# Performance work log

Hardware: AMD Instinct MI355X
Metric: run time of the kernel (lower is better)

## Reference

```python
import jax, jax.numpy as jnp
from jax import lax
import numpy as np

B, L_IN, C_IN, C_MARK = 4, 1024, 7, 4
D, H, DK, DFF, NL = 512, 8, 64, 2048, 4
WINDOW = [4, 4, 4]
INNER = 5


def _get_mask(input_size, window_size, inner_size):
    all_size = [input_size]
    for w in window_size:
        all_size.append(all_size[-1] // w)
    L = sum(all_size)
    m = np.zeros((L, L), dtype=np.float32)
    iw = inner_size // 2
    for li in range(len(all_size)):
        start = sum(all_size[:li])
        for i in range(start, start + all_size[li]):
            m[i, max(i - iw, start):min(i + iw + 1, start + all_size[li])] = 1
    for li in range(1, len(all_size)):
        start = sum(all_size[:li])
        for i in range(start, start + all_size[li]):
            ls = start - all_size[li - 1] + (i - start) * window_size[li - 1]
            if i == start + all_size[li] - 1:
                rs = start
            else:
                rs = start - all_size[li - 1] + (i - start + 1) * window_size[li - 1]
            m[i, ls:rs] = 1
            m[ls:rs, i] = 1
    return (1 - m).astype(bool), all_size


def _refer_points(all_sizes, window_size):
    n = all_sizes[0]
    idx = np.zeros((n, len(all_sizes)), dtype=np.int64)
    for i in range(n):
        idx[i, 0] = i
        former = i
        for j in range(1, len(all_sizes)):
            start = sum(all_sizes[:j])
            inner = former - (start - all_sizes[j - 1])
            former = start + min(inner // window_size[j - 1], all_sizes[j] - 1)
            idx[i, j] = former
    return idx


def _pos_emb(L, d):
    pos = np.arange(L, dtype=np.float32)[:, None]
    div = np.exp(np.arange(0, d, 2, dtype=np.float32) * (-np.log(10000.0) / d))
    pe = np.zeros((L, d), dtype=np.float32)
    pe[:, 0::2] = np.sin(pos * div)
    pe[:, 1::2] = np.cos(pos * div)
    return pe


def _ln(x, g, b, eps=1e-5):
    mu = x.mean(-1, keepdims=True)
    v = ((x - mu) ** 2).mean(-1, keepdims=True)
    return (x - mu) * lax.rsqrt(v + eps) * g + b


def setup_inputs() -> dict:
    key = jax.random.key(0)
    ks = iter(jax.random.split(key, 64))

    def nrm(shape, fan_in):
        return jax.random.normal(next(ks), shape, jnp.float32) / np.float32(np.sqrt(fan_in))

    return dict(
        x_enc=jax.random.normal(next(ks), (B, L_IN, C_IN), jnp.float32),
        x_mark=jax.random.uniform(next(ks), (B, L_IN, C_MARK), jnp.float32),
        conv_w=nrm((D, C_IN, 3), C_IN * 3), conv_b=jnp.zeros((D,), jnp.float32),
        temp_w=nrm((C_MARK, D), C_MARK), temp_b=jnp.zeros((D,), jnp.float32),
        down_w=nrm((D, DK), D), down_b=jnp.zeros((DK,), jnp.float32),
        pyr_conv_w=nrm((3, DK, DK, WINDOW[0]), DK * WINDOW[0]),
        pyr_conv_b=jnp.zeros((3, DK), jnp.float32),
        bn_g=jnp.ones((3, DK), jnp.float32), bn_b=jnp.zeros((3, DK), jnp.float32),
        up_w=nrm((DK, D), DK), up_b=jnp.zeros((D,), jnp.float32),
        norm_g=jnp.ones((D,), jnp.float32), norm_b=jnp.zeros((D,), jnp.float32),
        wq=nrm((NL, D, H * DK), D), wk=nrm((NL, D, H * DK), D), wv=nrm((NL, D, H * DK), D),
        fc_w=nrm((NL, H * DK, D), H * DK), fc_b=jnp.zeros((NL, D), jnp.float32),
        ln1_g=jnp.ones((NL, D), jnp.float32), ln1_b=jnp.zeros((NL, D), jnp.float32),
        w1=nrm((NL, D, DFF), D), b1=jnp.zeros((NL, DFF), jnp.float32),
        w2=nrm((NL, DFF, D), DFF), b2=jnp.zeros((NL, D), jnp.float32),
        ln2_g=jnp.ones((NL, D), jnp.float32), ln2_b=jnp.zeros((NL, D), jnp.float32),
    )


def reference(x_enc, x_mark, conv_w, conv_b, temp_w, temp_b, down_w, down_b,
              pyr_conv_w, pyr_conv_b, bn_g, bn_b, up_w, up_b, norm_g, norm_b,
              wq, wk, wv, fc_w, fc_b, ln1_g, ln1_b, w1, b1, w2, b2, ln2_g, ln2_b):
    mask_np, all_size = _get_mask(L_IN, WINDOW, INNER)
    mask = jnp.asarray(mask_np)                      # (L_tot, L_tot) bool, True = blocked
    idx = jnp.asarray(_refer_points(all_size, WINDOW))  # (L_IN, n_levels)
    pe = jnp.asarray(_pos_emb(L_IN, D))
    L_tot = sum(all_size)

    # --- DataEmbedding: circular Conv1d token emb + positional + temporal linear ---
    xt = jnp.transpose(x_enc, (0, 2, 1))             # (B, C_IN, L)
    xt = jnp.concatenate([xt[:, :, -1:], xt, xt[:, :, :1]], axis=-1)  # circular pad=1
    val = lax.conv_general_dilated(xt, conv_w, (1,), 'VALID',
                                   dimension_numbers=('NCH', 'OIH', 'NCH'))
    val = jnp.transpose(val, (0, 2, 1)) + conv_b
    seq = val + pe[None] + x_mark @ temp_w + temp_b  # (B, L_IN, D); dropout = eval no-op

    # --- Bottleneck_Construct: build pyramid levels with strided convs ---
    tmp = jnp.transpose(seq @ down_w + down_b, (0, 2, 1))  # (B, DK, L_IN)
    outs = []
    for i in range(len(WINDOW)):
        tmp = lax.conv_general_dilated(tmp, pyr_conv_w[i], (WINDOW[i],), 'VALID',
                                       dimension_numbers=('NCH', 'OIH', 'NCH'))
        tmp = tmp + pyr_conv_b[i][None, :, None]
        # BatchNorm1d at eval with running stats (0,1): affine only
        tmp = jax.nn.elu(tmp * bn_g[i][None, :, None] + bn_b[i][None, :, None])
        outs.append(tmp)
    pyr = jnp.transpose(jnp.concatenate(outs, axis=2), (0, 2, 1)) @ up_w + up_b
    seq = _ln(jnp.concatenate([seq, pyr], axis=1), norm_g, norm_b)  # (B, L_tot, D)

    temperature = float(np.sqrt(DK))
    for l in range(NL):
        # post-norm multi-head attention with pyramidal boolean mask
        res = seq
        q = (seq @ wq[l]).reshape(B, L_tot, H, DK)
        k = (seq @ wk[l]).reshape(B, L_tot, H, DK)
        v = (seq @ wv[l]).reshape(B, L_tot, H, DK)
        att = jnp.einsum('bqhd,bkhd->bhqk', q / temperature, k)
        att = jnp.where(mask[None, None], jnp.float32(-1e9), att)
        p = jax.nn.softmax(att, axis=-1)
        o = jnp.einsum('bhqk,bkhd->bqhd', p, v).reshape(B, L_tot, H * DK)
        seq = _ln(o @ fc_w[l] + fc_b[l] + res, ln1_g[l], ln1_b[l])
        # post-norm FFN (exact gelu, as F.gelu)
        res = seq
        hmid = jax.nn.gelu(seq @ w1[l] + b1[l], approximate=False)
        seq = _ln(hmid @ w2[l] + b2[l] + res, ln2_g[l], ln2_b[l])

    # --- refer_points gather: concat all pyramid levels per input position ---
    out = seq[:, idx, :]                             # (B, L_IN, n_levels, D)
    return out.reshape(B, L_IN, -1)                  # (B, L_IN, n_levels*D)
```

## Files before the change

### kernel.cpp

```cpp
#include <hip/hip_runtime.h>
#include <hip/hip_bf16.h>
#include <math.h>


typedef __attribute__((ext_vector_type(8))) short short8;
typedef __attribute__((ext_vector_type(4))) float f32x4;

__device__ inline ushort f2bf(float x) {
  union { __hip_bfloat16 h; ushort u; } cv; cv.h = __float2bfloat16(x); return cv.u;
}
__device__ inline float bf2f(ushort u) {
  union { unsigned int i; float f; } cv; cv.i = (unsigned)u << 16; return cv.f;
}
__device__ inline float lo16(unsigned u) { union { unsigned i; float f; } c; c.i = u << 16; return c.f; }
__device__ inline float hi16(unsigned u) { union { unsigned i; float f; } c; c.i = u & 0xffff0000u; return c.f; }

__device__ inline float gelu_f(float x) {
  float y = 0.7978845608028654f * (x + 0.044715f * x * x * x);
  float t = __expf(-2.0f * y);
  float th = (1.0f - t) / (1.0f + t);
  return 0.5f * x * (1.0f + th);
}

__device__ inline int xcd_chunk(int orig, int nwg) {
  int q = nwg >> 3, r = nwg & 7;
  int xcd = orig & 7, idx = orig >> 3;
  int base = (xcd < r) ? xcd * (q + 1) : r * (q + 1) + (xcd - r) * q;
  return base + idx;
}

#define GLD16(gp, lp)                                                        \
  __builtin_amdgcn_global_load_lds(                                          \
      (const __attribute__((address_space(1))) void*)(gp),                   \
      (__attribute__((address_space(3))) void*)(lp), 16, 0, 0)

__global__ __launch_bounds__(512) void embed_kernel(
    const float* __restrict__ x_enc, const float* __restrict__ x_mark,
    const float* __restrict__ conv_w, const float* __restrict__ conv_b,
    const float* __restrict__ temp_w, const float* __restrict__ temp_b,
    float* __restrict__ e) {
  int bl = blockIdx.x;
  int b = bl >> 10, l = bl & 1023;
  int d = threadIdx.x;
  int lm1 = (l + 1023) & 1023;
  int lp1 = (l + 1) & 1023;
  const float* w  = conv_w + d * 21;
  const float* x0 = x_enc + (size_t)(b * 1024 + lm1) * 7;
  const float* x1 = x_enc + (size_t)(b * 1024 + l)   * 7;
  const float* x2 = x_enc + (size_t)(b * 1024 + lp1) * 7;
  float acc = conv_b[d];
#pragma unroll
  for (int ci = 0; ci < 7; ci++) {
    acc = fmaf(x0[ci], w[ci * 3 + 0], acc);
    acc = fmaf(x1[ci], w[ci * 3 + 1], acc);
    acc = fmaf(x2[ci], w[ci * 3 + 2], acc);
  }
  int j = d >> 1;
  float dv = expf((float)(2 * j) * (-9.210340371976184f / 512.0f));
  float ang = (float)l * dv;
  float pe = (d & 1) ? cosf(ang) : sinf(ang);
  const float* xm = x_mark + (size_t)(b * 1024 + l) * 4;
  float mk = temp_b[d];
  mk = fmaf(xm[0], temp_w[d],        mk);
  mk = fmaf(xm[1], temp_w[512 + d],  mk);
  mk = fmaf(xm[2], temp_w[1024 + d], mk);
  mk = fmaf(xm[3], temp_w[1536 + d], mk);
  e[(size_t)bl * 512 + d] = acc + pe + mk;
}

__global__ __launch_bounds__(256) void transpose_cast(
    const float* __restrict__ src, ushort* __restrict__ dst,
    int K, int N, size_t src_lstride, size_t dst_lstride) {
  src += (size_t)blockIdx.z * src_lstride;
  dst += (size_t)blockIdx.z * dst_lstride;
  __shared__ float t[32][33];
  int k0 = blockIdx.y * 32, n0 = blockIdx.x * 32;
  int tx = threadIdx.x, ty = threadIdx.y;
#pragma unroll
  for (int i = 0; i < 4; i++)
    t[ty + i * 8][tx] = src[(size_t)(k0 + ty + i * 8) * N + n0 + tx];
  __syncthreads();
#pragma unroll
  for (int i = 0; i < 4; i++)
    dst[(size_t)(n0 + ty + i * 8) * K + k0 + tx] = f2bf(t[tx][ty + i * 8]);
}

__global__ __launch_bounds__(256) void gemm_bf16(
    const ushort* __restrict__ A, const ushort* __restrict__ Bt,
    const float* __restrict__ bias, void* __restrict__ C,
    int N, int K, int act, int out_bf16) {
  __shared__ short As[2][4096];
  __shared__ short Bs[2][8192];
  int nbx = N >> 7;
  int wgid = xcd_chunk(blockIdx.x, gridDim.x);
  int bx = wgid % nbx, by = wgid / nbx;
  int tid = threadIdx.x;
  int w = tid >> 6, lane = tid & 63;
  int bm = by << 6, bn = bx << 7;
  int gch = (tid & 7) ^ ((tid >> 3) & 7);
  const short* Ab = (const short*)A + (size_t)(bm + (tid >> 3)) * K + gch * 8;
  const short* Bb = (const short*)Bt + (size_t)(bn + (tid >> 3)) * K + gch * 8;
  int ldst = (tid & 192) * 8;
  int wr = (w >> 1) << 5, wc = (w & 1) << 6;
  int lr = lane & 15, kg = lane >> 4;
  int cs0 = ((kg)     ^ (lane & 7)) * 8;
  int cs1 = ((4 + kg) ^ (lane & 7)) * 8;
  f32x4 acc[2][4] = {};
#define STG(buf, kt)  do {                                                   \
    GLD16(Ab + (kt),                      &As[buf][ldst]);                   \
    GLD16(Ab + (kt) + (size_t)32 * K,     &As[buf][2048 + ldst]);            \
    GLD16(Bb + (kt),                      &Bs[buf][ldst]);                   \
    GLD16(Bb + (kt) + (size_t)32 * K,     &Bs[buf][2048 + ldst]);            \
    GLD16(Bb + (kt) + (size_t)64 * K,     &Bs[buf][4096 + ldst]);            \
    GLD16(Bb + (kt) + (size_t)96 * K,     &Bs[buf][6144 + ldst]); } while (0)
  STG(0, 0);
  __syncthreads();
  int nt = K >> 6;
  for (int t = 0; t < nt; t++) {
    int cur = t & 1;
    if (t + 1 < nt) STG(cur ^ 1, (t + 1) << 6);
    short8 a_[2][2], b_[4][2];
#pragma unroll
    for (int m = 0; m < 2; m++) {
      int rb = (wr + m * 16 + lr) * 64;
      a_[m][0] = *(const short8*)&As[cur][rb + cs0];
      a_[m][1] = *(const short8*)&As[cur][rb + cs1];
    }
#pragma unroll
    for (int n = 0; n < 4; n++) {
      int rb = (wc + n * 16 + lr) * 64;
      b_[n][0] = *(const short8*)&Bs[cur][rb + cs0];
      b_[n][1] = *(const short8*)&Bs[cur][rb + cs1];
    }
#pragma unroll
    for (int ks = 0; ks < 2; ks++)
#pragma unroll
      for (int m = 0; m < 2; m++)
#pragma unroll
        for (int n = 0; n < 4; n++)
          acc[m][n] = __builtin_amdgcn_mfma_f32_16x16x32_bf16(a_[m][ks], b_[n][ks], acc[m][n], 0, 0, 0);
    __syncthreads();
  }
#undef STG
  int r0 = bm + wr + kg * 4;
  int c0 = bn + wc + lr;
#pragma unroll
  for (int m = 0; m < 2; m++) {
#pragma unroll
    for (int n = 0; n < 4; n++) {
      int col = c0 + n * 16;
      float bv = bias ? bias[col] : 0.0f;
#pragma unroll
      for (int j = 0; j < 4; j++) {
        int row = r0 + m * 16 + j;
        float v = acc[m][n][j] + bv;
        if (act == 1) v = gelu_f(v);
        if (out_bf16) ((ushort*)C)[(size_t)row * N + col] = f2bf(v);
        else          ((float*)C)[(size_t)row * N + col] = v;
      }
    }
  }
}

__global__ __launch_bounds__(256) void gemm_bf16_t64(
    const ushort* __restrict__ A, const ushort* __restrict__ Bt,
    const float* __restrict__ bias, void* __restrict__ C,
    int N, int K, int out_bf16) {
  __shared__ short As[2][4096];
  __shared__ short Bs[2][4096];
  int nbx = N >> 6;
  int wgid = xcd_chunk(blockIdx.x, gridDim.x);
  int bx = wgid % nbx, by = wgid / nbx;
  int tid = threadIdx.x;
  int w = tid >> 6, lane = tid & 63;
  int bm = by << 6, bn = bx << 6;
  int gch = (tid & 7) ^ ((tid >> 3) & 7);
  const short* Ab = (const short*)A + (size_t)(bm + (tid >> 3)) * K + gch * 8;
  const short* Bb = (const short*)Bt + (size_t)(bn + (tid >> 3)) * K + gch * 8;
  int ldst = (tid & 192) * 8;
  int wr = (w >> 1) << 5, wc = (w & 1) << 5;
  int lr = lane & 15, kg = lane >> 4;
  int cs0 = ((kg)     ^ (lane & 7)) * 8;
  int cs1 = ((4 + kg) ^ (lane & 7)) * 8;
  f32x4 acc[2][2] = {};
#define STG64(buf, kt) do {                                                  \
    GLD16(Ab + (kt),                  &As[buf][ldst]);                       \
    GLD16(Ab + (kt) + (size_t)32 * K, &As[buf][2048 + ldst]);                \
    GLD16(Bb + (kt),                  &Bs[buf][ldst]);                       \
    GLD16(Bb + (kt) + (size_t)32 * K, &Bs[buf][2048 + ldst]); } while (0)
  STG64(0, 0);
  __syncthreads();
  int nt = K >> 6;
  for (int t = 0; t < nt; t++) {
    int cur = t & 1;
    if (t + 1 < nt) STG64(cur ^ 1, (t + 1) << 6);
    short8 a_[2][2], b_[2][2];
#pragma unroll
    for (int m = 0; m < 2; m++) {
      int rb = (wr + m * 16 + lr) * 64;
      a_[m][0] = *(const short8*)&As[cur][rb + cs0];
      a_[m][1] = *(const short8*)&As[cur][rb + cs1];
    }
#pragma unroll
    for (int n = 0; n < 2; n++) {
      int rb = (wc + n * 16 + lr) * 64;
      b_[n][0] = *(const short8*)&Bs[cur][rb + cs0];
      b_[n][1] = *(const short8*)&Bs[cur][rb + cs1];
    }
#pragma unroll
    for (int ks = 0; ks < 2; ks++)
#pragma unroll
      for (int m = 0; m < 2; m++)
#pragma unroll
        for (int n = 0; n < 2; n++)
          acc[m][n] = __builtin_amdgcn_mfma_f32_16x16x32_bf16(a_[m][ks], b_[n][ks], acc[m][n], 0, 0, 0);
    __syncthreads();
  }
#undef STG64
  int r0 = bm + wr + kg * 4;
  int c0 = bn + wc + lr;
#pragma unroll
  for (int m = 0; m < 2; m++) {
#pragma unroll
    for (int n = 0; n < 2; n++) {
      int col = c0 + n * 16;
      float bv = bias ? bias[col] : 0.0f;
#pragma unroll
      for (int j = 0; j < 4; j++) {
        int row = r0 + m * 16 + j;
        float v = acc[m][n][j] + bv;
        if (out_bf16) ((ushort*)C)[(size_t)row * N + col] = f2bf(v);
        else          ((float*)C)[(size_t)row * N + col] = v;
      }
    }
  }
}

__global__ __launch_bounds__(256) void down_gemm(
    const float* __restrict__ A, const float* __restrict__ B,
    const float* __restrict__ bias, float* __restrict__ C) {
  int wgid = xcd_chunk(blockIdx.x, gridDim.x);
  int r0 = wgid << 4;
  int tid = threadIdx.x;
  int col = tid & 63, rq = tid >> 6;
  __shared__ float As[16][32];
  __shared__ float Bs[32][64];
  float acc0 = 0, acc1 = 0, acc2 = 0, acc3 = 0;
  for (int kt = 0; kt < 512; kt += 32) {
    {
      int e = tid * 2;
      int ar = e >> 5, ak = e & 31;
      *(float2*)&As[ar][ak] = *(const float2*)&A[(size_t)(r0 + ar) * 512 + kt + ak];
    }
    {
      int e = tid * 8;
      int br = e >> 6, bc = e & 63;
      *(float4*)&Bs[br][bc]     = *(const float4*)&B[(size_t)(kt + br) * 64 + bc];
      *(float4*)&Bs[br][bc + 4] = *(const float4*)&B[(size_t)(kt + br) * 64 + bc + 4];
    }
    __syncthreads();
#pragma unroll
    for (int kk = 0; kk < 32; kk++) {
      float bv = Bs[kk][col];
      acc0 = fmaf(As[rq][kk],      bv, acc0);
      acc1 = fmaf(As[rq + 4][kk],  bv, acc1);
      acc2 = fmaf(As[rq + 8][kk],  bv, acc2);
      acc3 = fmaf(As[rq + 12][kk], bv, acc3);
    }
    __syncthreads();
  }
  float bv = bias[col];
  C[(size_t)(r0 + rq) * 64 + col]      = acc0 + bv;
  C[(size_t)(r0 + rq + 4) * 64 + col]  = acc1 + bv;
  C[(size_t)(r0 + rq + 8) * 64 + col]  = acc2 + bv;
  C[(size_t)(r0 + rq + 12) * 64 + col] = acc3 + bv;
}

__global__ __launch_bounds__(256) void gemm_f32(
    const float* __restrict__ A, const float* __restrict__ B,
    const float* __restrict__ bias, float* __restrict__ C,
    int M, int N, int K) {
  __shared__ float As[16][68];
  __shared__ float Bs[16][64];
  int tid = threadIdx.x;
  int tx = tid & 15, ty = tid >> 4;
  int bm = blockIdx.y << 6, bn = blockIdx.x << 6;
  const float* Ab = A + (size_t)bm * K;
  const float* Bb = B + bn;
  float acc[4][4] = {};
  for (int kt = 0; kt < K; kt += 16) {
#pragma unroll
    for (int r = 0; r < 4; r++) {
      int e2 = r * 256 + tid;
      As[e2 & 15][e2 >> 4] = Ab[(size_t)(e2 >> 4) * K + kt + (e2 & 15)];
    }
#pragma unroll
    for (int r = 0; r < 4; r++) {
      int e2 = r * 256 + tid;
      Bs[e2 >> 6][e2 & 63] = Bb[(size_t)(kt + (e2 >> 6)) * N + (e2 & 63)];
    }
    __syncthreads();
#pragma unroll
    for (int kk = 0; kk < 16; kk++) {
      float a0 = As[kk][(ty << 2) + 0], a1 = As[kk][(ty << 2) + 1];
      float a2 = As[kk][(ty << 2) + 2], a3 = As[kk][(ty << 2) + 3];
      float b0 = Bs[kk][(tx << 2) + 0], b1 = Bs[kk][(tx << 2) + 1];
      float b2 = Bs[kk][(tx << 2) + 2], b3 = Bs[kk][(tx << 2) + 3];
      acc[0][0] = fmaf(a0, b0, acc[0][0]); acc[0][1] = fmaf(a0, b1, acc[0][1]);
      acc[0][2] = fmaf(a0, b2, acc[0][2]); acc[0][3] = fmaf(a0, b3, acc[0][3]);
      acc[1][0] = fmaf(a1, b0, acc[1][0]); acc[1][1] = fmaf(a1, b1, acc[1][1]);
      acc[1][2] = fmaf(a1, b2, acc[1][2]); acc[1][3] = fmaf(a1, b3, acc[1][3]);
      acc[2][0] = fmaf(a2, b0, acc[2][0]); acc[2][1] = fmaf(a2, b1, acc[2][1]);
      acc[2][2] = fmaf(a2, b2, acc[2][2]); acc[2][3] = fmaf(a2, b3, acc[2][3]);
      acc[3][0] = fmaf(a3, b0, acc[3][0]); acc[3][1] = fmaf(a3, b1, acc[3][1]);
      acc[3][2] = fmaf(a3, b2, acc[3][2]); acc[3][3] = fmaf(a3, b3, acc[3][3]);
    }
    __syncthreads();
  }
#pragma unroll
  for (int i2 = 0; i2 < 4; i2++) {
    int row = bm + (ty << 2) + i2;
#pragma unroll
    for (int j2 = 0; j2 < 4; j2++) {
      int col = bn + (tx << 2) + j2;
      C[(size_t)row * N + col] = acc[i2][j2] + (bias ? bias[col] : 0.0f);
    }
  }
}

__global__ __launch_bounds__(64) void pyr_conv(
    const float* __restrict__ in, int in_base, int in_bstr,
    float* __restrict__ out, int out_base, int out_bstr, int out_len,
    const float* __restrict__ w, const float* __restrict__ bias,
    const float* __restrict__ bng, const float* __restrict__ bnb) {
  int blk = blockIdx.x;
  int b = blk / out_len, to = blk - b * out_len;
  int co = threadIdx.x;
  __shared__ float xin[4][64];
  const float* src = in + (size_t)(b * in_bstr + in_base + 4 * to) * 64;
#pragma unroll
  for (int r2 = 0; r2 < 4; r2++) xin[r2][co] = src[r2 * 64 + co];
  __syncthreads();
  const float* wr = w + (size_t)co * 256;
  float acc = bias[co];
#pragma unroll 16
  for (int ci = 0; ci < 64; ci++) {
    acc = fmaf(xin[0][ci], wr[ci * 4 + 0], acc);
    acc = fmaf(xin[1][ci], wr[ci * 4 + 1], acc);
    acc = fmaf(xin[2][ci], wr[ci * 4 + 2], acc);
    acc = fmaf(xin[3][ci], wr[ci * 4 + 3], acc);
  }
  float y = fmaf(bng[co], acc, bnb[co]);
  y = y > 0.0f ? y : expm1f(y);
  out[(size_t)(b * out_bstr + out_base + to) * 64 + co] = y;
}

__global__ __launch_bounds__(256) void ln_concat(
    const float* __restrict__ e, const float* __restrict__ pyru,
    const float* __restrict__ g, const float* __restrict__ bta,
    float* __restrict__ seq, ushort* __restrict__ seq_bf) {
  int r = blockIdx.x;
  int b = r / 1360, i = r - b * 1360;
  int tid = threadIdx.x;
  const float* src = (i < 1024)
      ? (e    + (size_t)(b * 1024 + i) * 512)
      : (pyru + (size_t)(b * 336 + (i - 1024)) * 512);
  float v0 = src[tid], v1 = src[tid + 256];
  __shared__ float red[256];
  red[tid] = v0 + v1;
  __syncthreads();
  for (int st = 128; st > 0; st >>= 1) { if (tid < st) red[tid] += red[tid + st]; __syncthreads(); }
  float mu = red[0] * (1.0f / 512.0f);
  __syncthreads();
  float d0 = v0 - mu, d1 = v1 - mu;
  red[tid] = d0 * d0 + d1 * d1;
  __syncthreads();
  for (int st = 128; st > 0; st >>= 1) { if (tid < st) red[tid] += red[tid + st]; __syncthreads(); }
  float inv = rsqrtf(red[0] * (1.0f / 512.0f) + 1e-5f);
  float o0 = d0 * inv * g[tid]       + bta[tid];
  float o1 = d1 * inv * g[tid + 256] + bta[tid + 256];
  float* dst = seq + (size_t)r * 512;
  dst[tid] = o0; dst[tid + 256] = o1;
  ushort* dbf = seq_bf + (size_t)r * 512;
  dbf[tid] = f2bf(o0); dbf[tid + 256] = f2bf(o1);
}

__global__ __launch_bounds__(256) void ln_add(
    float* __restrict__ seq, const ushort* __restrict__ t1,
    const float* __restrict__ g, const float* __restrict__ bta,
    ushort* __restrict__ seq_bf) {
  int r = blockIdx.x;
  int tid = threadIdx.x;
  float* row = seq + (size_t)r * 512;
  const ushort* trow = t1 + (size_t)r * 512;
  float v0 = row[tid] + bf2f(trow[tid]);
  float v1 = row[tid + 256] + bf2f(trow[tid + 256]);
  __shared__ float red[256];
  red[tid] = v0 + v1;
  __syncthreads();
  for (int st = 128; st > 0; st >>= 1) { if (tid < st) red[tid] += red[tid + st]; __syncthreads(); }
  float mu = red[0] * (1.0f / 512.0f);
  __syncthreads();
  float d0 = v0 - mu, d1 = v1 - mu;
  red[tid] = d0 * d0 + d1 * d1;
  __syncthreads();
  for (int st = 128; st > 0; st >>= 1) { if (tid < st) red[tid] += red[tid + st]; __syncthreads(); }
  float inv = rsqrtf(red[0] * (1.0f / 512.0f) + 1e-5f);
  float o0 = d0 * inv * g[tid]       + bta[tid];
  float o1 = d1 * inv * g[tid + 256] + bta[tid + 256];
  row[tid] = o0; row[tid + 256] = o1;
  ushort* dbf = seq_bf + (size_t)r * 512;
  dbf[tid] = f2bf(o0); dbf[tid + 256] = f2bf(o1);
}

__global__ __launch_bounds__(512) void attn_sparse(
    const ushort* __restrict__ qkv, ushort* __restrict__ o) {
  int r = blockIdx.x;
  int b = r / 1360, i = r - b * 1360;
  int h = threadIdx.x >> 6, lane = threadIdx.x & 63;
  int S, sz, li;
  if (i < 1024)      { li = 0; S = 0;    sz = 1024; }
  else if (i < 1280) { li = 1; S = 1024; sz = 256; }
  else if (i < 1344) { li = 2; S = 1280; sz = 64; }
  else               { li = 3; S = 1344; sz = 16; }
  int p = i - S;
  int lo = p - 2; if (lo < 0) lo = 0;
  int hi = p + 2; if (hi > sz - 1) hi = sz - 1;
  int cnt = hi - lo + 1;
  int nk = cnt + (li > 0 ? 4 : 0) + (li < 3 ? 1 : 0);
  int Sprev = (li == 1) ? 0 : (li == 2) ? 1024 : 1280;
  int Snext = (li == 0) ? 1024 : (li == 1) ? 1280 : 1344;
  int j2 = lane >> 2, c = lane & 3;
  int key;
  if (j2 < cnt)                      key = S + lo + j2;
  else if (li > 0 && j2 - cnt < 4)   key = Sprev + 4 * p + (j2 - cnt);
  else if (li < 3)                   key = Snext + (p >> 2);
  else                               key = S + p;
  float partial = 0.0f;
  {
    const uint4* qv = (const uint4*)(qkv + (size_t)r * 1536 + h * 64 + c * 16);
    const uint4* kv = (const uint4*)(qkv + (size_t)(b * 1360 + key) * 1536 + 512 + h * 64 + c * 16);
#pragma unroll
    for (int cc = 0; cc < 2; cc++) {
      uint4 a = qv[cc], k4 = kv[cc];
      partial = fmaf(lo16(a.x), lo16(k4.x), partial); partial = fmaf(hi16(a.x), hi16(k4.x), partial);
      partial = fmaf(lo16(a.y), lo16(k4.y), partial); partial = fmaf(hi16(a.y), hi16(k4.y), partial);
      partial = fmaf(lo16(a.z), lo16(k4.z), partial); partial = fmaf(hi16(a.z), hi16(k4.z), partial);
      partial = fmaf(lo16(a.w), lo16(k4.w), partial); partial = fmaf(hi16(a.w), hi16(k4.w), partial);
    }
  }
  partial += __shfl_xor(partial, 1);
  partial += __shfl_xor(partial, 2);
  float s = partial * 0.125f;
  float m = -1e30f;
  for (int j = 0; j < nk; j++) m = fmaxf(m, __shfl(s, 4 * j));
  float denom = 0.0f;
  for (int j = 0; j < nk; j++) denom += __expf(__shfl(s, 4 * j) - m);
  float inv = 1.0f / denom;
  float acc = 0.0f;
  for (int j = 0; j < nk; j++) {
    float pj = __expf(__shfl(s, 4 * j) - m) * inv;
    int kj = __shfl(key, 4 * j);
    float vv = bf2f(qkv[(size_t)(b * 1360 + kj) * 1536 + 1024 + h * 64 + lane]);
    acc = fmaf(pj, vv, acc);
  }
  o[(size_t)r * 512 + h * 64 + lane] = f2bf(acc);
}

__global__ __launch_bounds__(512) void gather_out(
    const float* __restrict__ seq, float* __restrict__ out) {
  int bl = blockIdx.x;
  int b = bl >> 10, i = bl & 1023;
  int d = threadIdx.x;
  size_t ob = (size_t)bl * 2048 + d;
  size_t base = (size_t)b * 1360;
  out[ob]        = seq[(base + i) * 512 + d];
  out[ob + 512]  = seq[(base + 1024 + (i >> 2)) * 512 + d];
  out[ob + 1024] = seq[(base + 1280 + (i >> 4)) * 512 + d];
  out[ob + 1536] = seq[(base + 1344 + (i >> 6)) * 512 + d];
}

extern "C" void kernel_launch(void* const* d_in, const int* in_sizes, int n_in,
                              void* d_out, int out_size, void* d_ws, size_t ws_size,
                              hipStream_t stream) {
  const float* x_enc   = (const float*)d_in[0];
  const float* x_mark  = (const float*)d_in[1];
  const float* conv_w  = (const float*)d_in[2];
  const float* conv_b  = (const float*)d_in[3];
  const float* temp_w  = (const float*)d_in[4];
  const float* temp_b  = (const float*)d_in[5];
  const float* down_w  = (const float*)d_in[6];
  const float* down_b  = (const float*)d_in[7];
  const float* pyr_w   = (const float*)d_in[8];
  const float* pyr_b   = (const float*)d_in[9];
  const float* bn_g    = (const float*)d_in[10];
  const float* bn_b    = (const float*)d_in[11];
  const float* up_w    = (const float*)d_in[12];
  const float* up_b    = (const float*)d_in[13];
  const float* norm_g  = (const float*)d_in[14];
  const float* norm_b  = (const float*)d_in[15];
  const float* wq      = (const float*)d_in[16];
  const float* wk      = (const float*)d_in[17];
  const float* wv      = (const float*)d_in[18];
  const float* fc_w    = (const float*)d_in[19];
  const float* fc_b    = (const float*)d_in[20];
  const float* ln1_g   = (const float*)d_in[21];
  const float* ln1_b   = (const float*)d_in[22];
  const float* w1      = (const float*)d_in[23];
  const float* b1      = (const float*)d_in[24];
  const float* w2      = (const float*)d_in[25];
  const float* b2      = (const float*)d_in[26];
  const float* ln2_g   = (const float*)d_in[27];
  const float* ln2_b   = (const float*)d_in[28];

  float* ws = (float*)d_ws;
  float*  e      = ws;
  float*  tmp0   = ws + 2097152;
  float*  pyrf   = ws + 2359296;
  float*  pyru   = ws + 2445312;
  ushort* qkv_bf = (ushort*)ws;
  ushort* o_bf   = (ushort*)(ws + 4227072);
  ushort* th_bf  = (ushort*)ws;
  ushort* t1     = (ushort*)(ws + 5636096);
  float*  seq    = ws + 8454144;
  ushort* seq_bf = (ushort*)(ws + 11272192);
  ushort* qkvw   = (ushort*)(ws + 12681216);
  ushort* fcw    = (ushort*)(ws + 14254080);
  ushort* w1t    = (ushort*)(ws + 14778368);
  ushort* w2t    = (ushort*)(ws + 16875520);

  dim3 tb(32, 8);
  transpose_cast<<<dim3(16, 16, 4), tb, 0, stream>>>(wq, qkvw,          512, 512,  262144, 786432);
  transpose_cast<<<dim3(16, 16, 4), tb, 0, stream>>>(wk, qkvw + 262144, 512, 512,  262144, 786432);
  transpose_cast<<<dim3(16, 16, 4), tb, 0, stream>>>(wv, qkvw + 524288, 512, 512,  262144, 786432);
  transpose_cast<<<dim3(16, 16, 4), tb, 0, stream>>>(fc_w, fcw,         512, 512,  262144, 262144);
  transpose_cast<<<dim3(64, 16, 4), tb, 0, stream>>>(w1, w1t,           512, 2048, 1048576, 1048576);
  transpose_cast<<<dim3(16, 64, 4), tb, 0, stream>>>(w2, w2t,           2048, 512, 1048576, 1048576);

  embed_kernel<<<4096, 512, 0, stream>>>(x_enc, x_mark, conv_w, conv_b,
                                         temp_w, temp_b, e);
  down_gemm<<<256, 256, 0, stream>>>(e, down_w, down_b, tmp0);
  pyr_conv<<<4 * 256, 64, 0, stream>>>(tmp0, 0, 1024, pyrf, 0, 336, 256,
                                       pyr_w, pyr_b, bn_g, bn_b);
  pyr_conv<<<4 * 64, 64, 0, stream>>>(pyrf, 0, 336, pyrf, 256, 336, 64,
                                      pyr_w + 16384, pyr_b + 64, bn_g + 64, bn_b + 64);
  pyr_conv<<<4 * 16, 64, 0, stream>>>(pyrf, 256, 336, pyrf, 320, 336, 16,
                                      pyr_w + 32768, pyr_b + 128, bn_g + 128, bn_b + 128);
  gemm_f32<<<dim3(8, 21), 256, 0, stream>>>(pyrf, up_w, up_b, pyru, 1344, 512, 64);
  ln_concat<<<5440, 256, 0, stream>>>(e, pyru, norm_g, norm_b, seq, seq_bf);

  for (int l = 0; l < 4; l++) {
    gemm_bf16<<<12 * 86, 256, 0, stream>>>(seq_bf, qkvw + (size_t)l * 786432,
                                           nullptr, qkv_bf, 1536, 512, 0, 1);
    attn_sparse<<<5440, 512, 0, stream>>>(qkv_bf, o_bf);
    gemm_bf16_t64<<<8 * 86, 256, 0, stream>>>(o_bf, fcw + (size_t)l * 262144,
                                              fc_b + l * 512, t1, 512, 512, 1);
    ln_add<<<5440, 256, 0, stream>>>(seq, t1, ln1_g + l * 512, ln1_b + l * 512, seq_bf);
    gemm_bf16<<<16 * 86, 256, 0, stream>>>(seq_bf, w1t + (size_t)l * 1048576,
                                           b1 + l * 2048, th_bf, 2048, 512, 1, 1);
    gemm_bf16_t64<<<8 * 86, 256, 0, stream>>>(th_bf, w2t + (size_t)l * 1048576,
                                              b2 + l * 512, t1, 512, 2048, 1);
    ln_add<<<5440, 256, 0, stream>>>(seq, t1, ln2_g + l * 512, ln2_b + l * 512, seq_bf);
  }
  gather_out<<<4096, 512, 0, stream>>>(seq, (float*)d_out);
}
```

Baseline: 619.6 us.

## Use 32-row tiles for N=512 GEMMs and wave-per-row layernorm kernels

The output-projection and FFN-down GEMMs now use a 32x64 tile instead of 64x64, doubling the workgroup count from 688 to 1376 so the GPU's compute units are better filled. The layernorm kernels now assign one 64-lane wave per row, using float4/uint4 vector loads and shuffle reductions in place of shared-memory tree reductions with many barriers. The smaller tile reloads the B operand more often per output element, and each wave does more serial work per row.

```diff
diff --git a/kernel.cpp b/kernel.cpp
--- a/kernel.cpp
+++ b/kernel.cpp
@@ -14,6 +14,9 @@
 }
 __device__ inline float lo16(unsigned u) { union { unsigned i; float f; } c; c.i = u << 16; return c.f; }
 __device__ inline float hi16(unsigned u) { union { unsigned i; float f; } c; c.i = u & 0xffff0000u; return c.f; }
+__device__ inline unsigned pack2(float a, float b) {
+  return (unsigned)f2bf(a) | ((unsigned)f2bf(b) << 16);
+}
 
 __device__ inline float gelu_f(float x) {
   float y = 0.7978845608028654f * (x + 0.044715f * x * x * x);
@@ -162,44 +165,42 @@
   }
 }
 
-__global__ __launch_bounds__(256) void gemm_bf16_t64(
+__global__ __launch_bounds__(256) void gemm_bf16_t32(
     const ushort* __restrict__ A, const ushort* __restrict__ Bt,
-    const float* __restrict__ bias, void* __restrict__ C,
-    int N, int K, int out_bf16) {
-  __shared__ short As[2][4096];
+    const float* __restrict__ bias, ushort* __restrict__ C,
+    int N, int K) {
+  __shared__ short As[2][2048];
   __shared__ short Bs[2][4096];
   int nbx = N >> 6;
   int wgid = xcd_chunk(blockIdx.x, gridDim.x);
   int bx = wgid % nbx, by = wgid / nbx;
   int tid = threadIdx.x;
   int w = tid >> 6, lane = tid & 63;
-  int bm = by << 6, bn = bx << 6;
+  int bm = by << 5, bn = bx << 6;
   int gch = (tid & 7) ^ ((tid >> 3) & 7);
   const short* Ab = (const short*)A + (size_t)(bm + (tid >> 3)) * K + gch * 8;
   const short* Bb = (const short*)Bt + (size_t)(bn + (tid >> 3)) * K + gch * 8;
   int ldst = (tid & 192) * 8;
-  int wr = (w >> 1) << 5, wc = (w & 1) << 5;
+  int wr = (w >> 1) << 4, wc = (w & 1) << 5;
   int lr = lane & 15, kg = lane >> 4;
   int cs0 = ((kg)     ^ (lane & 7)) * 8;
   int cs1 = ((4 + kg) ^ (lane & 7)) * 8;
-  f32x4 acc[2][2] = {};
-#define STG64(buf, kt) do {                                                  \
+  f32x4 acc[2] = {};
+#define STG32(buf, kt) do {                                                  \
     GLD16(Ab + (kt),                  &As[buf][ldst]);                       \
-    GLD16(Ab + (kt) + (size_t)32 * K, &As[buf][2048 + ldst]);                \
     GLD16(Bb + (kt),                  &Bs[buf][ldst]);                       \
     GLD16(Bb + (kt) + (size_t)32 * K, &Bs[buf][2048 + ldst]); } while (0)
-  STG64(0, 0);
+  STG32(0, 0);
   __syncthreads();
   int nt = K >> 6;
   for (int t = 0; t < nt; t++) {
     int cur = t & 1;
-    if (t + 1 < nt) STG64(cur ^ 1, (t + 1) << 6);
-    short8 a_[2][2], b_[2][2];
-#pragma unroll
-    for (int m = 0; m < 2; m++) {
-      int rb = (wr + m * 16 + lr) * 64;
-      a_[m][0] = *(const short8*)&As[cur][rb + cs0];
-      a_[m][1] = *(const short8*)&As[cur][rb + cs1];
+    if (t + 1 < nt) STG32(cur ^ 1, (t + 1) << 6);
+    short8 a_[2], b_[2][2];
+    {
+      int rb = (wr + lr) * 64;
+      a_[0] = *(const short8*)&As[cur][rb + cs0];
+      a_[1] = *(const short8*)&As[cur][rb + cs1];
     }
 #pragma unroll
     for (int n = 0; n < 2; n++) {
@@ -210,28 +211,21 @@
 #pragma unroll
     for (int ks = 0; ks < 2; ks++)
 #pragma unroll
-      for (int m = 0; m < 2; m++)
-#pragma unroll
-        for (int n = 0; n < 2; n++)
-          acc[m][n] = __builtin_amdgcn_mfma_f32_16x16x32_bf16(a_[m][ks], b_[n][ks], acc[m][n], 0, 0, 0);
+      for (int n = 0; n < 2; n++)
+        acc[n] = __builtin_amdgcn_mfma_f32_16x16x32_bf16(a_[ks], b_[n][ks], acc[n], 0, 0, 0);
     __syncthreads();
   }
-#undef STG64
+#undef STG32
   int r0 = bm + wr + kg * 4;
   int c0 = bn + wc + lr;
 #pragma unroll
-  for (int m = 0; m < 2; m++) {
-#pragma unroll
-    for (int n = 0; n < 2; n++) {
-      int col = c0 + n * 16;
-      float bv = bias ? bias[col] : 0.0f;
-#pragma unroll
-      for (int j = 0; j < 4; j++) {
-        int row = r0 + m * 16 + j;
-        float v = acc[m][n][j] + bv;
-        if (out_bf16) ((ushort*)C)[(size_t)row * N + col] = f2bf(v);
-        else          ((float*)C)[(size_t)row * N + col] = v;
-      }
+  for (int n = 0; n < 2; n++) {
+    int col = c0 + n * 16;
+    float bv = bias ? bias[col] : 0.0f;
+#pragma unroll
+    for (int j = 0; j < 4; j++) {
+      int row = r0 + j;
+      C[(size_t)row * N + col] = f2bf(acc[n][j] + bv);
     }
   }
 }
@@ -359,58 +353,79 @@
     const float* __restrict__ e, const float* __restrict__ pyru,
     const float* __restrict__ g, const float* __restrict__ bta,
     float* __restrict__ seq, ushort* __restrict__ seq_bf) {
-  int r = blockIdx.x;
+  int r = (blockIdx.x << 2) + (threadIdx.x >> 6);
+  int lane = threadIdx.x & 63;
   int b = r / 1360, i = r - b * 1360;
-  int tid = threadIdx.x;
   const float* src = (i < 1024)
       ? (e    + (size_t)(b * 1024 + i) * 512)
       : (pyru + (size_t)(b * 336 + (i - 1024)) * 512);
-  float v0 = src[tid], v1 = src[tid + 256];
-  __shared__ float red[256];
-  red[tid] = v0 + v1;
-  __syncthreads();
-  for (int st = 128; st > 0; st >>= 1) { if (tid < st) red[tid] += red[tid + st]; __syncthreads(); }
-  float mu = red[0] * (1.0f / 512.0f);
-  __syncthreads();
-  float d0 = v0 - mu, d1 = v1 - mu;
-  red[tid] = d0 * d0 + d1 * d1;
-  __syncthreads();
-  for (int st = 128; st > 0; st >>= 1) { if (tid < st) red[tid] += red[tid + st]; __syncthreads(); }
-  float inv = rsqrtf(red[0] * (1.0f / 512.0f) + 1e-5f);
-  float o0 = d0 * inv * g[tid]       + bta[tid];
-  float o1 = d1 * inv * g[tid + 256] + bta[tid + 256];
-  float* dst = seq + (size_t)r * 512;
-  dst[tid] = o0; dst[tid + 256] = o1;
-  ushort* dbf = seq_bf + (size_t)r * 512;
-  dbf[tid] = f2bf(o0); dbf[tid + 256] = f2bf(o1);
+  int c = lane << 3;
+  float4 v0 = *(const float4*)&src[c];
+  float4 v1 = *(const float4*)&src[c + 4];
+  float sum = v0.x + v0.y + v0.z + v0.w + v1.x + v1.y + v1.z + v1.w;
+#pragma unroll
+  for (int off = 1; off < 64; off <<= 1) sum += __shfl_xor(sum, off);
+  float mu = sum * (1.0f / 512.0f);
+  float d[8] = { v0.x - mu, v0.y - mu, v0.z - mu, v0.w - mu,
+                 v1.x - mu, v1.y - mu, v1.z - mu, v1.w - mu };
+  float sq = d[0]*d[0] + d[1]*d[1] + d[2]*d[2] + d[3]*d[3]
+           + d[4]*d[4] + d[5]*d[5] + d[6]*d[6] + d[7]*d[7];
+#pragma unroll
+  for (int off = 1; off < 64; off <<= 1) sq += __shfl_xor(sq, off);
+  float inv = rsqrtf(sq * (1.0f / 512.0f) + 1e-5f);
+  float4 g0 = *(const float4*)&g[c],   g1 = *(const float4*)&g[c + 4];
+  float4 b0 = *(const float4*)&bta[c], b1 = *(const float4*)&bta[c + 4];
+  float o[8] = { d[0]*inv*g0.x + b0.x, d[1]*inv*g0.y + b0.y,
+                 d[2]*inv*g0.z + b0.z, d[3]*inv*g0.w + b0.w,
+                 d[4]*inv*g1.x + b1.x, d[5]*inv*g1.y + b1.y,
+                 d[6]*inv*g1.z + b1.z, d[7]*inv*g1.w + b1.w };
+  float* dst = seq + (size_t)r * 512 + c;
+  *(float4*)&dst[0] = make_float4(o[0], o[1], o[2], o[3]);
+  *(float4*)&dst[4] = make_float4(o[4], o[5], o[6], o[7]);
+  uint4 pk;
+  pk.x = pack2(o[0], o[1]); pk.y = pack2(o[2], o[3]);
+  pk.z = pack2(o[4], o[5]); pk.w = pack2(o[6], o[7]);
+  *(uint4*)(seq_bf + (size_t)r * 512 + c) = pk;
 }
 
 __global__ __launch_bounds__(256) void ln_add(
     float* __restrict__ seq, const ushort* __restrict__ t1,
     const float* __restrict__ g, const float* __restrict__ bta,
     ushort* __restrict__ seq_bf) {
-  int r = blockIdx.x;
-  int tid = threadIdx.x;
-  float* row = seq + (size_t)r * 512;
-  const ushort* trow = t1 + (size_t)r * 512;
-  float v0 = row[tid] + bf2f(trow[tid]);
-  float v1 = row[tid + 256] + bf2f(trow[tid + 256]);
-  __shared__ float red[256];
-  red[tid] = v0 + v1;
-  __syncthreads();
-  for (int st = 128; st > 0; st >>= 1) { if (tid < st) red[tid] += red[tid + st]; __syncthreads(); }
-  float mu = red[0] * (1.0f / 512.0f);
-  __syncthreads();
-  float d0 = v0 - mu, d1 = v1 - mu;
-  red[tid] = d0 * d0 + d1 * d1;
-  __syncthreads();
-  for (int st = 128; st > 0; st >>= 1) { if (tid < st) red[tid] += red[tid + st]; __syncthreads(); }
-  float inv = rsqrtf(red[0] * (1.0f / 512.0f) + 1e-5f);
-  float o0 = d0 * inv * g[tid]       + bta[tid];
-  float o1 = d1 * inv * g[tid + 256] + bta[tid + 256];
-  row[tid] = o0; row[tid + 256] = o1;
-  ushort* dbf = seq_bf + (size_t)r * 512;
-  dbf[tid] = f2bf(o0); dbf[tid + 256] = f2bf(o1);
+  int r = (blockIdx.x << 2) + (threadIdx.x >> 6);
+  int lane = threadIdx.x & 63;
+  int c = lane << 3;
+  float* row = seq + (size_t)r * 512 + c;
+  float4 v0 = *(const float4*)&row[0];
+  float4 v1 = *(const float4*)&row[4];
+  uint4 tv = *(const uint4*)(t1 + (size_t)r * 512 + c);
+  v0.x += lo16(tv.x); v0.y += hi16(tv.x);
+  v0.z += lo16(tv.y); v0.w += hi16(tv.y);
+  v1.x += lo16(tv.z); v1.y += hi16(tv.z);
+  v1.z += lo16(tv.w); v1.w += hi16(tv.w);
+  float sum = v0.x + v0.y + v0.z + v0.w + v1.x + v1.y + v1.z + v1.w;
+#pragma unroll
+  for (int off = 1; off < 64; off <<= 1) sum += __shfl_xor(sum, off);
+  float mu = sum * (1.0f / 512.0f);
+  float d[8] = { v0.x - mu, v0.y - mu, v0.z - mu, v0.w - mu,
+                 v1.x - mu, v1.y - mu, v1.z - mu, v1.w - mu };
+  float sq = d[0]*d[0] + d[1]*d[1] + d[2]*d[2] + d[3]*d[3]
+           + d[4]*d[4] + d[5]*d[5] + d[6]*d[6] + d[7]*d[7];
+#pragma unroll
+  for (int off = 1; off < 64; off <<= 1) sq += __shfl_xor(sq, off);
+  float inv = rsqrtf(sq * (1.0f / 512.0f) + 1e-5f);
+  float4 g0 = *(const float4*)&g[c],   g1 = *(const float4*)&g[c + 4];
+  float4 b0 = *(const float4*)&bta[c], b1 = *(const float4*)&bta[c + 4];
+  float o[8] = { d[0]*inv*g0.x + b0.x, d[1]*inv*g0.y + b0.y,
+                 d[2]*inv*g0.z + b0.z, d[3]*inv*g0.w + b0.w,
+                 d[4]*inv*g1.x + b1.x, d[5]*inv*g1.y + b1.y,
+                 d[6]*inv*g1.z + b1.z, d[7]*inv*g1.w + b1.w };
+  *(float4*)&row[0] = make_float4(o[0], o[1], o[2], o[3]);
+  *(float4*)&row[4] = make_float4(o[4], o[5], o[6], o[7]);
+  uint4 pk;
+  pk.x = pack2(o[0], o[1]); pk.y = pack2(o[2], o[3]);
+  pk.z = pack2(o[4], o[5]); pk.w = pack2(o[6], o[7]);
+  *(uint4*)(seq_bf + (size_t)r * 512 + c) = pk;
 }
 
 __global__ __launch_bounds__(512) void attn_sparse(
@@ -547,20 +562,20 @@
   pyr_conv<<<4 * 16, 64, 0, stream>>>(pyrf, 256, 336, pyrf, 320, 336, 16,
                                       pyr_w + 32768, pyr_b + 128, bn_g + 128, bn_b + 128);
   gemm_f32<<<dim3(8, 21), 256, 0, stream>>>(pyrf, up_w, up_b, pyru, 1344, 512, 64);
-  ln_concat<<<5440, 256, 0, stream>>>(e, pyru, norm_g, norm_b, seq, seq_bf);
+  ln_concat<<<1360, 256, 0, stream>>>(e, pyru, norm_g, norm_b, seq, seq_bf);
 
   for (int l = 0; l < 4; l++) {
     gemm_bf16<<<12 * 86, 256, 0, stream>>>(seq_bf, qkvw + (size_t)l * 786432,
                                            nullptr, qkv_bf, 1536, 512, 0, 1);
     attn_sparse<<<5440, 512, 0, stream>>>(qkv_bf, o_bf);
-    gemm_bf16_t64<<<8 * 86, 256, 0, stream>>>(o_bf, fcw + (size_t)l * 262144,
-                                              fc_b + l * 512, t1, 512, 512, 1);
-    ln_add<<<5440, 256, 0, stream>>>(seq, t1, ln1_g + l * 512, ln1_b + l * 512, seq_bf);
+    gemm_bf16_t32<<<8 * 172, 256, 0, stream>>>(o_bf, fcw + (size_t)l * 262144,
+                                               fc_b + l * 512, t1, 512, 512);
+    ln_add<<<1360, 256, 0, stream>>>(seq, t1, ln1_g + l * 512, ln1_b + l * 512, seq_bf);
     gemm_bf16<<<16 * 86, 256, 0, stream>>>(seq_bf, w1t + (size_t)l * 1048576,
                                            b1 + l * 2048, th_bf, 2048, 512, 1, 1);
-    gemm_bf16_t64<<<8 * 86, 256, 0, stream>>>(th_bf, w2t + (size_t)l * 1048576,
-                                              b2 + l * 512, t1, 512, 2048, 1);
-    ln_add<<<5440, 256, 0, stream>>>(seq, t1, ln2_g + l * 512, ln2_b + l * 512, seq_bf);
+    gemm_bf16_t32<<<8 * 172, 256, 0, stream>>>(th_bf, w2t + (size_t)l * 1048576,
+                                               b2 + l * 512, t1, 512, 2048);
+    ln_add<<<1360, 256, 0, stream>>>(seq, t1, ln2_g + l * 512, ln2_b + l * 512, seq_bf);
   }
   gather_out<<<4096, 512, 0, stream>>>(seq, (float*)d_out);
 }
```

Measured after the change: 609.2 us. Within noise of the previous version (-1.7%).
